# Kernel tuning notes

Hardware: AMD Instinct MI355X
Metric: run time of the kernel (lower is better)

The kernel has to match this reference:

```python
import jax, jax.numpy as jnp
import numpy as np

N = 65536   # total nodes
E = 262144  # total edges (before self loops)
B = 2048    # graphs in batch
H = 4       # attention heads
D = 192     # per-head dim (hidden_dim // heads)
HID = 768   # hidden dim
L = 2       # num layers
EPS = 1e-5
NEG_SLOPE = 0.2  # PyG GATConv leaky_relu slope


def setup_inputs() -> dict:
    key = jax.random.key(0)
    ks = jax.random.split(key, 10)
    s = 0.02
    x = jax.random.normal(ks[0], (N, HID), dtype=jnp.float32)
    edge_index = jax.random.randint(ks[1], (2, E), 0, N)
    batch_vec = jnp.sort(jax.random.randint(ks[2], (N,), 0, B))
    W = jax.random.normal(ks[3], (L, HID, HID), dtype=jnp.float32) * s
    att_src = jax.random.normal(ks[4], (L, H, D), dtype=jnp.float32) * s
    att_dst = jax.random.normal(ks[5], (L, H, D), dtype=jnp.float32) * s
    bias = jnp.zeros((L, HID), dtype=jnp.float32)
    ln_gamma = jnp.ones((L, HID), dtype=jnp.float32)
    ln_beta = jnp.zeros((L, HID), dtype=jnp.float32)
    out_w = jax.random.normal(ks[6], (HID, HID), dtype=jnp.float32) * s
    out_b = jnp.zeros((HID,), dtype=jnp.float32)
    return dict(x=x, edge_index=edge_index, batch_vec=batch_vec, W=W,
                att_src=att_src, att_dst=att_dst, bias=bias,
                ln_gamma=ln_gamma, ln_beta=ln_beta, out_w=out_w, out_b=out_b)


def _gat_layer(x, src, dst, W_l, a_src, a_dst, b_l):
    # x: [N, HID] -> projected per-head features [N, H, D]
    xw = (x @ W_l).reshape(N, H, D)
    alpha_src = jnp.einsum('nhd,hd->nh', xw, a_src)  # [N, H]
    alpha_dst = jnp.einsum('nhd,hd->nh', xw, a_dst)  # [N, H]
    # edge attention logits (message j->i uses alpha_src[j] + alpha_dst[i])
    e = jax.nn.leaky_relu(alpha_src[src] + alpha_dst[dst], NEG_SLOPE)  # [E2, H]
    # segment softmax over incoming edges per destination node (self loops
    # guarantee every node has >= 1 incoming edge)
    m = jax.ops.segment_max(e, dst, num_segments=N)
    ex = jnp.exp(e - m[dst])
    denom = jax.ops.segment_sum(ex, dst, num_segments=N)
    alpha = ex / denom[dst]                                            # [E2, H]
    # attention-weighted scatter aggregation
    out = jax.ops.segment_sum(alpha[:, :, None] * xw[src], dst, num_segments=N)
    return out.reshape(N, HID) + b_l


def reference(x, edge_index, batch_vec, W, att_src, att_dst, bias,
              ln_gamma, ln_beta, out_w, out_b):
    loops = jnp.arange(N)
    src = jnp.concatenate([edge_index[0], loops])  # add_self_loops=True
    dst = jnp.concatenate([edge_index[1], loops])
    h = x
    for l in range(L):
        out = _gat_layer(h, src, dst, W[l], att_src[l], att_dst[l], bias[l])
        mu = jnp.mean(out, axis=-1, keepdims=True)
        var = jnp.var(out, axis=-1, keepdims=True)
        out = (out - mu) * jax.lax.rsqrt(var + EPS) * ln_gamma[l] + ln_beta[l]
        out = jax.nn.relu(out)
        h = out + h  # residual (in_dim == hidden_dim for every layer)
    # global mean pool over graphs
    ones = jnp.ones((N,), h.dtype)
    cnt = jax.ops.segment_sum(ones, batch_vec, num_segments=B)
    h_g = jax.ops.segment_sum(h, batch_vec, num_segments=B)
    h_g = h_g / jnp.maximum(cnt, 1.0)[:, None]
    return h_g @ out_w + out_b
```

## Files before the change

### kernel.cpp

```cpp
#include <hip/hip_runtime.h>
#include <hip/hip_bf16.h>

constexpr int NN  = 65536;
constexpr int EE  = 262144;
constexpr int E2  = EE + NN;
constexpr int BB  = 2048;
constexpr int HH  = 4;
constexpr int DD  = 192;
constexpr int HD  = 768;
constexpr int LL  = 2;
constexpr float EPS = 1e-5f;
constexpr float SLOPE = 0.2f;

typedef __attribute__((ext_vector_type(8))) short short8;
typedef __attribute__((ext_vector_type(4))) float f32x4;
typedef __hip_bfloat16 bf16;

__global__ void zero_k(float* __restrict__ p, int n) {
    int i = blockIdx.x * 256 + threadIdx.x;
    if (i < n) p[i] = 0.f;
}

__global__ void conv_k(const float4* __restrict__ src, bf16* __restrict__ dst, int n4) {
    int i = blockIdx.x * 256 + threadIdx.x;
    if (i >= n4) return;
    float4 v = src[i];
    bf16* o = dst + (size_t)i * 4;
    o[0] = __float2bfloat16(v.x); o[1] = __float2bfloat16(v.y);
    o[2] = __float2bfloat16(v.z); o[3] = __float2bfloat16(v.w);
}

__global__ __launch_bounds__(256) void wconv3_k(const float* __restrict__ W,
                                                const float* __restrict__ OW,
                                                bf16* __restrict__ Wt3) {
    __shared__ float tile[32][33];
    const float* src = (blockIdx.z < 2) ? (W + (size_t)blockIdx.z * HD * HD) : OW;
    bf16* dst = Wt3 + (size_t)blockIdx.z * HD * HD;
    int bx = blockIdx.x * 32;
    int by = blockIdx.y * 32;
    int tx = threadIdx.x & 31, ty = threadIdx.x >> 5;
    #pragma unroll
    for (int r = 0; r < 32; r += 8)
        tile[ty + r][tx] = src[(size_t)(by + ty + r) * HD + bx + tx];
    __syncthreads();
    #pragma unroll
    for (int r = 0; r < 32; r += 8)
        dst[(size_t)(bx + ty + r) * HD + by + tx] = __float2bfloat16(tile[tx][ty + r]);
}

__device__ __forceinline__ void load16_lds(const void* g, void* l) {
    __builtin_amdgcn_global_load_lds(
        (const __attribute__((address_space(1))) unsigned int*)g,
        (__attribute__((address_space(3))) unsigned int*)l, 16, 0, 0);
}

template <bool BF16_OUT, bool SWIZ>
__global__ __launch_bounds__(256) void gemm_bf16_k(
    const bf16* __restrict__ A, const bf16* __restrict__ Bt,
    float* __restrict__ Cf, bf16* __restrict__ Cb, const float* __restrict__ bias)
{
    constexpr int K = HD;
    __shared__ __attribute__((aligned(16))) short As[128 * 32];
    __shared__ __attribute__((aligned(16))) short Bs[128 * 32];

    int bx, by;
    if (SWIZ) {
        int gid = blockIdx.x;
        int xcd = gid & 7, lid = gid >> 3;
        int sg = lid / 48, sl = lid - sg * 48;
        by = (xcd << 6) + (sg << 3) + (sl & 7);
        bx = sl >> 3;
    } else {
        bx = blockIdx.x; by = blockIdx.y;
    }

    int tid  = threadIdx.x;
    int wave = tid >> 6, lane = tid & 63;
    int wy = wave >> 1, wx = wave & 1;
    int m16 = lane & 15, quad = lane >> 4;
    int bm = by * 128;
    int bn = bx * 128;

    int p0 = wave * 128 + lane;
    int r0 = p0 >> 2, c0 = p0 & 3;
    int p1 = p0 + 64;
    int r1 = p1 >> 2, c1 = p1 & 3;

    const bf16* gA0 = A  + (size_t)(bm + r0) * K + c0 * 8;
    const bf16* gA1 = A  + (size_t)(bm + r1) * K + c1 * 8;
    const bf16* gB0 = Bt + (size_t)(bn + r0) * K + c0 * 8;
    const bf16* gB1 = Bt + (size_t)(bn + r1) * K + c1 * 8;

    f32x4 acc[4][4];
    #pragma unroll
    for (int i = 0; i < 4; i++)
        #pragma unroll
        for (int j = 0; j < 4; j++) acc[i][j] = (f32x4)0.f;

    const short8* Ac = (const short8*)As;
    const short8* Bc = (const short8*)Bs;

    for (int k0 = 0; k0 < K; k0 += 32) {
        load16_lds(gA0 + k0, &As[p0 * 8]);
        load16_lds(gA1 + k0, &As[p1 * 8]);
        load16_lds(gB0 + k0, &Bs[p0 * 8]);
        load16_lds(gB1 + k0, &Bs[p1 * 8]);
        __syncthreads();

        short8 a[4], b[4];
        #pragma unroll
        for (int i = 0; i < 4; i++)
            a[i] = Ac[(wy * 64 + i * 16 + m16) * 4 + quad];
        #pragma unroll
        for (int j = 0; j < 4; j++)
            b[j] = Bc[(wx * 64 + j * 16 + m16) * 4 + quad];
        #pragma unroll
        for (int i = 0; i < 4; i++)
            #pragma unroll
            for (int j = 0; j < 4; j++)
                acc[i][j] = __builtin_amdgcn_mfma_f32_16x16x32_bf16(a[i], b[j], acc[i][j], 0, 0, 0);
        __syncthreads();
    }

    #pragma unroll
    for (int j = 0; j < 4; j++) {
        int col = bn + wx * 64 + j * 16 + m16;
        float badd = (!BF16_OUT && bias) ? bias[col] : 0.f;
        #pragma unroll
        for (int i = 0; i < 4; i++) {
            int row0 = bm + wy * 64 + i * 16 + quad * 4;
            #pragma unroll
            for (int r = 0; r < 4; r++) {
                if (BF16_OUT)
                    Cb[(size_t)(row0 + r) * HD + col] = __float2bfloat16(acc[i][j][r]);
                else
                    Cf[(size_t)(row0 + r) * HD + col] = acc[i][j][r] + badd;
            }
        }
    }
}

__device__ __forceinline__ float bflo(unsigned u) { return __uint_as_float(u << 16); }
__device__ __forceinline__ float bfhi(unsigned u) { return __uint_as_float(u & 0xffff0000u); }

__global__ __launch_bounds__(256) void alpha_k(
    const bf16* __restrict__ xw,
    const float* __restrict__ asl, const float* __restrict__ adl,
    float* __restrict__ asrc, float* __restrict__ adst)
{
    int n = blockIdx.x, t = threadIdx.x;
    int head = t >> 6, lane = t & 63;
    float s1 = 0.f, s2 = 0.f;
    if (lane < 48) {
        int c = head * DD + lane * 4;
        uint2 u = *(const uint2*)(xw + (size_t)n * HD + c);
        float4 a1 = *(const float4*)(asl + c);
        float4 a2 = *(const float4*)(adl + c);
        float v0 = bflo(u.x), v1 = bfhi(u.x), v2 = bflo(u.y), v3 = bfhi(u.y);
        s1 = v0 * a1.x + v1 * a1.y + v2 * a1.z + v3 * a1.w;
        s2 = v0 * a2.x + v1 * a2.y + v2 * a2.z + v3 * a2.w;
    }
    #pragma unroll
    for (int off = 32; off > 0; off >>= 1) {
        s1 += __shfl_down(s1, off, 64);
        s2 += __shfl_down(s2, off, 64);
    }
    if (lane == 0) {
        asrc[(size_t)n * HH + head] = s1;
        adst[(size_t)n * HH + head] = s2;
    }
}

__global__ void hist_k(const int* __restrict__ ei, int* __restrict__ deg) {
    int e = blockIdx.x * 256 + threadIdx.x;
    int dst = (e < EE) ? ei[EE + e] : (e - EE);
    atomicAdd(&deg[dst], 1);
}

__global__ void scan1_k(const int* __restrict__ deg, int* __restrict__ incl,
                        int* __restrict__ blocksum) {
    __shared__ int s[256];
    int t = threadIdx.x, n = blockIdx.x * 256 + t;
    int v = deg[n];
    s[t] = v;
    for (int off = 1; off < 256; off <<= 1) {
        __syncthreads();
        int tmp = (t >= off) ? s[t - off] : 0;
        __syncthreads();
        s[t] += tmp;
    }
    incl[n] = s[t];
    if (t == 255) blocksum[blockIdx.x] = s[255];
}

__global__ void scan2_k(const int* __restrict__ blocksum, int* __restrict__ blockoff) {
    __shared__ int s[256];
    int t = threadIdx.x;
    int v = blocksum[t];
    s[t] = v;
    for (int off = 1; off < 256; off <<= 1) {
        __syncthreads();
        int tmp = (t >= off) ? s[t - off] : 0;
        __syncthreads();
        s[t] += tmp;
    }
    blockoff[t] = s[t] - v;
}

__global__ void scan3_k(const int* __restrict__ deg, const int* __restrict__ blockoff,
                        int* __restrict__ incl_cursor, int* __restrict__ rowstart) {
    int t = threadIdx.x, n = blockIdx.x * 256 + t;
    int rs = blockoff[blockIdx.x] + incl_cursor[n] - deg[n];
    rowstart[n] = rs;
    incl_cursor[n] = rs;
    if (n == 0) rowstart[NN] = E2;
}

__global__ void fill_k(const int* __restrict__ ei, int* __restrict__ cursor,
                       int* __restrict__ csr_src) {
    int e = blockIdx.x * 256 + threadIdx.x;
    int src = (e < EE) ? ei[e] : (e - EE);
    int dst = (e < EE) ? ei[EE + e] : (e - EE);
    int pos = atomicAdd(&cursor[dst], 1);
    csr_src[pos] = src;
}

__global__ __launch_bounds__(256) void agg_k(
    const bf16* __restrict__ xw, const float4* __restrict__ asrc,
    const float4* __restrict__ adst, const int* __restrict__ rowstart,
    const int* __restrict__ csr_src,
    const float* __restrict__ bias_l, const float* __restrict__ gamma_l,
    const float* __restrict__ beta_l, const bf16* __restrict__ h_in,
    bf16* __restrict__ h_out)
{
    __shared__ float s_w[4][64][4];
    __shared__ int   s_src[4][64];

    int wave = threadIdx.x >> 6, lane = threadIdx.x & 63;
    int i = blockIdx.x * 4 + wave;
    int c = lane * 12;
    int myhead = lane >> 4;

    int r0 = rowstart[i], r1 = rowstart[i + 1];
    float4 ad = adst[i];

    float acc[12];
    #pragma unroll
    for (int k = 0; k < 12; k++) acc[k] = 0.f;
    float4 den = make_float4(0.f, 0.f, 0.f, 0.f);

    for (int base = r0; base < r1; base += 64) {
        int cnt = min(64, r1 - base);
        float4 w4 = make_float4(0.f, 0.f, 0.f, 0.f);
        if (lane < cnt) {
            int s = csr_src[base + lane];
            s_src[wave][lane] = s;
            float4 a = asrc[s];
            float t0 = a.x + ad.x; t0 = (t0 > 0.f) ? t0 : SLOPE * t0;
            float t1 = a.y + ad.y; t1 = (t1 > 0.f) ? t1 : SLOPE * t1;
            float t2 = a.z + ad.z; t2 = (t2 > 0.f) ? t2 : SLOPE * t2;
            float t3 = a.w + ad.w; t3 = (t3 > 0.f) ? t3 : SLOPE * t3;
            w4 = make_float4(__expf(t0), __expf(t1), __expf(t2), __expf(t3));
            *(float4*)&s_w[wave][lane][0] = w4;
        }
        den.x += w4.x; den.y += w4.y; den.z += w4.z; den.w += w4.w;
        for (int e = 0; e < cnt; e++) {
            int src = __builtin_amdgcn_readfirstlane(s_src[wave][e]);
            float wv = s_w[wave][e][myhead];
            const bf16* row = xw + (size_t)src * HD + c;
            uint2 u0 = *(const uint2*)(row);
            uint2 u1 = *(const uint2*)(row + 4);
            uint2 u2 = *(const uint2*)(row + 8);
            acc[0] += wv * bflo(u0.x); acc[1]  += wv * bfhi(u0.x);
            acc[2] += wv * bflo(u0.y); acc[3]  += wv * bfhi(u0.y);
            acc[4] += wv * bflo(u1.x); acc[5]  += wv * bfhi(u1.x);
            acc[6] += wv * bflo(u1.y); acc[7]  += wv * bfhi(u1.y);
            acc[8] += wv * bflo(u2.x); acc[9]  += wv * bfhi(u2.x);
            acc[10] += wv * bflo(u2.y); acc[11] += wv * bfhi(u2.y);
        }
    }

    #pragma unroll
    for (int off = 32; off > 0; off >>= 1) {
        den.x += __shfl_xor(den.x, off, 64);
        den.y += __shfl_xor(den.y, off, 64);
        den.z += __shfl_xor(den.z, off, 64);
        den.w += __shfl_xor(den.w, off, 64);
    }
    float deni = (myhead == 0) ? den.x : (myhead == 1) ? den.y
               : (myhead == 2) ? den.z : den.w;
    float inv = 1.f / deni;

    float4 b0 = *(const float4*)(bias_l + c);
    float4 b1 = *(const float4*)(bias_l + c + 4);
    float4 b2 = *(const float4*)(bias_l + c + 8);
    float v[12];
    v[0] = acc[0] * inv + b0.x; v[1]  = acc[1] * inv + b0.y;
    v[2] = acc[2] * inv + b0.z; v[3]  = acc[3] * inv + b0.w;
    v[4] = acc[4] * inv + b1.x; v[5]  = acc[5] * inv + b1.y;
    v[6] = acc[6] * inv + b1.z; v[7]  = acc[7] * inv + b1.w;
    v[8] = acc[8] * inv + b2.x; v[9]  = acc[9] * inv + b2.y;
    v[10] = acc[10] * inv + b2.z; v[11] = acc[11] * inv + b2.w;

    float s = 0.f;
    #pragma unroll
    for (int k = 0; k < 12; k++) s += v[k];
    #pragma unroll
    for (int off = 32; off > 0; off >>= 1) s += __shfl_xor(s, off, 64);
    float mean = s * (1.f / (float)HD);

    float q = 0.f;
    #pragma unroll
    for (int k = 0; k < 12; k++) { float d = v[k] - mean; q += d * d; }
    #pragma unroll
    for (int off = 32; off > 0; off >>= 1) q += __shfl_xor(q, off, 64);
    float rs = rsqrtf(q * (1.f / (float)HD) + EPS);

    float4 g0 = *(const float4*)(gamma_l + c);
    float4 g1 = *(const float4*)(gamma_l + c + 4);
    float4 g2 = *(const float4*)(gamma_l + c + 8);
    float4 e0 = *(const float4*)(beta_l + c);
    float4 e1 = *(const float4*)(beta_l + c + 4);
    float4 e2 = *(const float4*)(beta_l + c + 8);
    float gg[12] = {g0.x,g0.y,g0.z,g0.w,g1.x,g1.y,g1.z,g1.w,g2.x,g2.y,g2.z,g2.w};
    float bb[12] = {e0.x,e0.y,e0.z,e0.w,e1.x,e1.y,e1.z,e1.w,e2.x,e2.y,e2.z,e2.w};

    const bf16* hrow = h_in + (size_t)i * HD + c;
    uint2 hu0 = *(const uint2*)(hrow);
    uint2 hu1 = *(const uint2*)(hrow + 4);
    uint2 hu2 = *(const uint2*)(hrow + 8);
    float hres[12] = {bflo(hu0.x), bfhi(hu0.x), bflo(hu0.y), bfhi(hu0.y),
                      bflo(hu1.x), bfhi(hu1.x), bflo(hu1.y), bfhi(hu1.y),
                      bflo(hu2.x), bfhi(hu2.x), bflo(hu2.y), bfhi(hu2.y)};

    bf16 pk[12];
    #pragma unroll
    for (int k = 0; k < 12; k++) {
        float o = fmaxf((v[k] - mean) * rs * gg[k] + bb[k], 0.f) + hres[k];
        pk[k] = __float2bfloat16(o);
    }
    bf16* orow = h_out + (size_t)i * HD + c;
    *(uint2*)(orow)     = *(const uint2*)&pk[0];
    *(uint2*)(orow + 4) = *(const uint2*)&pk[4];
    *(uint2*)(orow + 8) = *(const uint2*)&pk[8];
}

__global__ __launch_bounds__(192) void pool_k(
    const bf16* __restrict__ h, const int* __restrict__ bv,
    bf16* __restrict__ hg)
{
    int g = blockIdx.x, t = threadIdx.x;
    int lo = 0, hi = NN;
    while (lo < hi) { int mid = (lo + hi) >> 1; if (bv[mid] < g) lo = mid + 1; else hi = mid; }
    int start = lo;
    hi = NN;
    while (lo < hi) { int mid = (lo + hi) >> 1; if (bv[mid] < g + 1) lo = mid + 1; else hi = mid; }
    int end = lo;
    int c = t * 4;
    float a0 = 0.f, a1 = 0.f, a2 = 0.f, a3 = 0.f;
    for (int n = start; n < end; n++) {
        uint2 u = *(const uint2*)(h + (size_t)n * HD + c);
        a0 += bflo(u.x); a1 += bfhi(u.x); a2 += bflo(u.y); a3 += bfhi(u.y);
    }
    float sc = 1.f / fmaxf((float)(end - start), 1.f);
    bf16 pk[4];
    pk[0] = __float2bfloat16(a0 * sc); pk[1] = __float2bfloat16(a1 * sc);
    pk[2] = __float2bfloat16(a2 * sc); pk[3] = __float2bfloat16(a3 * sc);
    *(uint2*)(hg + (size_t)g * HD + c) = *(const uint2*)pk;
}

extern "C" void kernel_launch(void* const* d_in, const int* in_sizes, int n_in,
                              void* d_out, int out_size, void* d_ws, size_t ws_size,
                              hipStream_t stream)
{
    (void)in_sizes; (void)n_in; (void)out_size; (void)ws_size;
    const float* x       = (const float*)d_in[0];
    const int*   ei      = (const int*)d_in[1];
    const int*   bv      = (const int*)d_in[2];
    const float* W       = (const float*)d_in[3];
    const float* att_src = (const float*)d_in[4];
    const float* att_dst = (const float*)d_in[5];
    const float* bias    = (const float*)d_in[6];
    const float* gamma   = (const float*)d_in[7];
    const float* beta    = (const float*)d_in[8];
    const float* out_w   = (const float*)d_in[9];
    const float* out_b   = (const float*)d_in[10];
    float* out = (float*)d_out;

    char* p = (char*)d_ws;
    size_t off = 0;
    auto take = [&](size_t bytes) -> char* {
        char* r = p + off;
        off = (off + bytes + 255) & ~(size_t)255;
        return r;
    };
    bf16* xw        = (bf16*)take((size_t)NN * HD * 2);
    bf16* hbf0      = (bf16*)take((size_t)NN * HD * 2);
    bf16* hbf1      = (bf16*)take((size_t)NN * HD * 2);
    bf16* Wt3       = (bf16*)take((size_t)3 * HD * HD * 2);
    float* asrc     = (float*)take((size_t)NN * HH * 4);
    float* adst     = (float*)take((size_t)NN * HH * 4);
    int*   deg      = (int*)take((size_t)NN * 4);
    int*   rowstart = (int*)take((size_t)(NN + 1) * 4);
    int*   cursor   = (int*)take((size_t)NN * 4);
    int*   blocksum = (int*)take(256 * 4);
    int*   blockoff = (int*)take(256 * 4);
    int*   csr_src  = (int*)take((size_t)E2 * 4);
    bf16*  hg       = (bf16*)take((size_t)BB * HD * 2);

    const int EB = E2 / 256;

    zero_k<<<NN / 256, 256, 0, stream>>>((float*)deg, NN);
    hist_k<<<EB, 256, 0, stream>>>(ei, deg);
    scan1_k<<<NN / 256, 256, 0, stream>>>(deg, cursor, blocksum);
    scan2_k<<<1, 256, 0, stream>>>(blocksum, blockoff);
    scan3_k<<<NN / 256, 256, 0, stream>>>(deg, blockoff, cursor, rowstart);
    fill_k<<<EB, 256, 0, stream>>>(ei, cursor, csr_src);

    conv_k<<<(NN * HD / 4 + 255) / 256, 256, 0, stream>>>((const float4*)x, hbf0, NN * HD / 4);
    wconv3_k<<<dim3(HD / 32, HD / 32, 3), 256, 0, stream>>>(W, out_w, Wt3);

    bf16* hin = hbf0;
    bf16* hout = hbf1;
    for (int l = 0; l < LL; l++) {
        gemm_bf16_k<true, true><<<3072, 256, 0, stream>>>(
            hin, Wt3 + (size_t)l * HD * HD, nullptr, xw, nullptr);
        alpha_k<<<NN, 256, 0, stream>>>(xw, att_src + (size_t)l * HH * DD,
                                        att_dst + (size_t)l * HH * DD, asrc, adst);
        agg_k<<<NN / 4, 256, 0, stream>>>(xw, (const float4*)asrc, (const float4*)adst,
                                          rowstart, csr_src,
                                          bias + (size_t)l * HD, gamma + (size_t)l * HD,
                                          beta + (size_t)l * HD, hin, hout);
        bf16* tmp = hin; hin = hout; hout = tmp;
    }

    pool_k<<<BB, 192, 0, stream>>>(hin, bv, hg);
    gemm_bf16_k<false, false><<<dim3(HD / 128, BB / 128), 256, 0, stream>>>(
        hg, Wt3 + (size_t)2 * HD * HD, out, nullptr, out_b);
}
```

Measured before the change: 885.7 us.

## Use 256x256-tile quad-buffered GEMM and one-wave-per-node alpha kernel

Replaces the per-layer 128x128 GEMM with a 256x256-tile, 512-thread kernel. It stages four K-slices in LDS through direct global-to-LDS loads, keeps three stages in flight and raises wave priority around the MFMA block. The aim is more operand reuse per LDS byte and better latency hiding for the N×768×768 projection. The alpha kernel now handles one node per wave (four per block), with each lane covering 12 channels and a 16-lane xor reduction, which removes the idle lanes and quarter-occupied blocks of the old version. The new GEMM uses 128KB of LDS and a large accumulator set, so occupancy and register spills are a risk.

```diff
diff --git a/kernel.cpp b/kernel.cpp
--- a/kernel.cpp
+++ b/kernel.cpp
@@ -54,6 +54,97 @@
         (__attribute__((address_space(3))) unsigned int*)l, 16, 0, 0);
 }
 
+__global__ __launch_bounds__(512, 2) void gemm256_k(
+    const bf16* __restrict__ A, const bf16* __restrict__ Bt, bf16* __restrict__ C)
+{
+    constexpr int K  = HD;
+    constexpr int NT = K / 32;
+
+    __shared__ __attribute__((aligned(16))) char smem[4 * 32768];
+
+    int bid  = blockIdx.x;
+    int flat = (bid & 7) * 96 + (bid >> 3);
+    int by   = flat / 3;
+    int bx   = flat - by * 3;
+    int bm   = by * 256, bn = bx * 256;
+
+    int tid  = threadIdx.x;
+    int wid  = tid >> 6, lane = tid & 63;
+    int wr   = wid >> 2, wc = wid & 3;
+    int m16  = lane & 15, quad = lane >> 4;
+
+    int prow = ((tid >> 6) << 4) | (tid & 15);
+    int slot = (tid >> 4) & 3;
+    const bf16* gA = A  + (size_t)(bm + prow) * K + slot * 8;
+    const bf16* gB = Bt + (size_t)(bn + prow) * K + slot * 8;
+    char* ldst = smem + tid * 16;
+
+    auto STAGE = [&](int t) {
+        char* d = ldst + (size_t)(t & 3) * 32768;
+        const bf16* a = gA + t * 32;
+        const bf16* b = gB + t * 32;
+        load16_lds(a,                  d);
+        load16_lds(a + (size_t)128*K,  d + 8192);
+        load16_lds(b,                  d + 16384);
+        load16_lds(b + (size_t)128*K,  d + 24576);
+    };
+
+    f32x4 acc[8][4];
+    #pragma unroll
+    for (int i = 0; i < 8; i++)
+        #pragma unroll
+        for (int j = 0; j < 4; j++) acc[i][j] = (f32x4)0.f;
+
+    auto COMPUTE = [&](int t) {
+        const char* ab = smem + (size_t)(t & 3) * 32768;
+        const char* bb = ab + 16384;
+        short8 a[8], b[4];
+        #pragma unroll
+        for (int n = 0; n < 4; ++n)
+            b[n] = *(const short8*)(bb + (wc * 4 + n) * 1024 + lane * 16);
+        #pragma unroll
+        for (int m = 0; m < 8; ++m)
+            a[m] = *(const short8*)(ab + (wr * 8 + m) * 1024 + lane * 16);
+        __builtin_amdgcn_s_setprio(1);
+        #pragma unroll
+        for (int m = 0; m < 8; ++m)
+            #pragma unroll
+            for (int n = 0; n < 4; ++n)
+                acc[m][n] = __builtin_amdgcn_mfma_f32_16x16x32_bf16(a[m], b[n], acc[m][n], 0, 0, 0);
+        __builtin_amdgcn_s_setprio(0);
+    };
+
+    STAGE(0); STAGE(1); STAGE(2);
+    asm volatile("s_waitcnt vmcnt(8)" ::: "memory");
+    __builtin_amdgcn_s_barrier();
+
+    for (int t = 0; t < NT - 3; ++t) {
+        STAGE(t + 3);
+        COMPUTE(t);
+        asm volatile("s_waitcnt vmcnt(8)" ::: "memory");
+        __builtin_amdgcn_s_barrier();
+    }
+    COMPUTE(NT - 3);
+    asm volatile("s_waitcnt vmcnt(4)" ::: "memory");
+    __builtin_amdgcn_s_barrier();
+    COMPUTE(NT - 2);
+    asm volatile("s_waitcnt vmcnt(0)" ::: "memory");
+    __builtin_amdgcn_s_barrier();
+    COMPUTE(NT - 1);
+
+    #pragma unroll
+    for (int m = 0; m < 8; ++m) {
+        int row0 = bm + wr * 128 + m * 16 + quad * 4;
+        #pragma unroll
+        for (int n = 0; n < 4; ++n) {
+            int col = bn + wc * 64 + n * 16 + m16;
+            #pragma unroll
+            for (int r = 0; r < 4; ++r)
+                C[(size_t)(row0 + r) * HD + col] = __float2bfloat16(acc[m][n][r]);
+        }
+    }
+}
+
 template <bool BF16_OUT, bool SWIZ>
 __global__ __launch_bounds__(256) void gemm_bf16_k(
     const bf16* __restrict__ A, const bf16* __restrict__ Bt,
@@ -148,24 +239,38 @@
     const float* __restrict__ asl, const float* __restrict__ adl,
     float* __restrict__ asrc, float* __restrict__ adst)
 {
-    int n = blockIdx.x, t = threadIdx.x;
-    int head = t >> 6, lane = t & 63;
+    int wave = threadIdx.x >> 6, lane = threadIdx.x & 63;
+    int n = blockIdx.x * 4 + wave;
+    int c = lane * 12;
+
+    const bf16* row = xw + (size_t)n * HD + c;
+    uint2 u0 = *(const uint2*)(row);
+    uint2 u1 = *(const uint2*)(row + 4);
+    uint2 u2 = *(const uint2*)(row + 8);
+    float v[12] = {bflo(u0.x), bfhi(u0.x), bflo(u0.y), bfhi(u0.y),
+                   bflo(u1.x), bfhi(u1.x), bflo(u1.y), bfhi(u1.y),
+                   bflo(u2.x), bfhi(u2.x), bflo(u2.y), bfhi(u2.y)};
+
+    float4 a0 = *(const float4*)(asl + c);
+    float4 a1 = *(const float4*)(asl + c + 4);
+    float4 a2 = *(const float4*)(asl + c + 8);
+    float4 d0 = *(const float4*)(adl + c);
+    float4 d1 = *(const float4*)(adl + c + 4);
+    float4 d2 = *(const float4*)(adl + c + 8);
+    float aa[12] = {a0.x,a0.y,a0.z,a0.w,a1.x,a1.y,a1.z,a1.w,a2.x,a2.y,a2.z,a2.w};
+    float dd[12] = {d0.x,d0.y,d0.z,d0.w,d1.x,d1.y,d1.z,d1.w,d2.x,d2.y,d2.z,d2.w};
+
     float s1 = 0.f, s2 = 0.f;
-    if (lane < 48) {
-        int c = head * DD + lane * 4;
-        uint2 u = *(const uint2*)(xw + (size_t)n * HD + c);
-        float4 a1 = *(const float4*)(asl + c);
-        float4 a2 = *(const float4*)(adl + c);
-        float v0 = bflo(u.x), v1 = bfhi(u.x), v2 = bflo(u.y), v3 = bfhi(u.y);
-        s1 = v0 * a1.x + v1 * a1.y + v2 * a1.z + v3 * a1.w;
-        s2 = v0 * a2.x + v1 * a2.y + v2 * a2.z + v3 * a2.w;
-    }
-    #pragma unroll
-    for (int off = 32; off > 0; off >>= 1) {
-        s1 += __shfl_down(s1, off, 64);
-        s2 += __shfl_down(s2, off, 64);
-    }
-    if (lane == 0) {
+    #pragma unroll
+    for (int k = 0; k < 12; k++) { s1 += v[k] * aa[k]; s2 += v[k] * dd[k]; }
+
+    #pragma unroll
+    for (int off = 1; off < 16; off <<= 1) {
+        s1 += __shfl_xor(s1, off, 64);
+        s2 += __shfl_xor(s2, off, 64);
+    }
+    if ((lane & 15) == 0) {
+        int head = lane >> 4;
         asrc[(size_t)n * HH + head] = s1;
         adst[(size_t)n * HH + head] = s2;
     }
@@ -423,10 +528,9 @@
     bf16* hin = hbf0;
     bf16* hout = hbf1;
     for (int l = 0; l < LL; l++) {
-        gemm_bf16_k<true, true><<<3072, 256, 0, stream>>>(
-            hin, Wt3 + (size_t)l * HD * HD, nullptr, xw, nullptr);
-        alpha_k<<<NN, 256, 0, stream>>>(xw, att_src + (size_t)l * HH * DD,
-                                        att_dst + (size_t)l * HH * DD, asrc, adst);
+        gemm256_k<<<768, 512, 0, stream>>>(hin, Wt3 + (size_t)l * HD * HD, xw);
+        alpha_k<<<NN / 4, 256, 0, stream>>>(xw, att_src + (size_t)l * HH * DD,
+                                            att_dst + (size_t)l * HH * DD, asrc, adst);
         agg_k<<<NN / 4, 256, 0, stream>>>(xw, (const float4*)asrc, (const float4*)adst,
                                           rowstart, csr_src,
                                           bias + (size_t)l * HD, gamma + (size_t)l * HD,
```

New measurement: 835.1 us. 1.06x faster.
